# Optimization experiments

Measured on AMD Instinct MI355X. Metric: run time of the kernel, lower is better.

The kernel has to match this reference:

```python
import jax, jax.numpy as jnp
import numpy as np

B, DIM, H, W = 8, 128, 112, 112
WSZ, K = 7, 9
D4 = DIM // 4


def setup_inputs() -> dict:
    key = jax.random.key(0)
    ks = jax.random.split(key, 8)
    w = lambda k, shape: jax.random.normal(k, shape, jnp.float32) * 0.05
    return {
        'x_in': jax.random.normal(ks[0], (B, DIM, H, W), jnp.float32),
        'f_w': w(ks[1], (D4, DIM)), 'f_b': jnp.zeros((D4,), jnp.float32),
        'f_gn_w': jnp.ones((D4,), jnp.float32), 'f_gn_b': jnp.zeros((D4,), jnp.float32),
        'p_w': w(ks[2], (DIM, D4)), 'p_b': jnp.zeros((DIM,), jnp.float32),
        'p_gn_w': jnp.ones((DIM,), jnp.float32), 'p_gn_b': jnp.zeros((DIM,), jnp.float32),
        'r_w': w(ks[3], (DIM, DIM)), 'r_b': jnp.zeros((DIM,), jnp.float32),
        'r_gn_w': jnp.ones((DIM,), jnp.float32), 'r_gn_b': jnp.zeros((DIM,), jnp.float32),
        'e1_w': w(ks[4], (D4, 2 * D4)), 'e1_b': jnp.zeros((D4,), jnp.float32),
        'e2_w': w(ks[5], (1, D4)), 'e2_b': jnp.zeros((1,), jnp.float32),
        'gamma': jnp.ones((1,), jnp.float32), 'beta': jnp.zeros((1,), jnp.float32),
    }


def conv1x1(x, w, b):
    # 1x1 conv == channel matmul. x: (B,C,H,W), w: (O,C)
    return jnp.einsum('bchw,oc->bohw', x, w) + b[None, :, None, None]


def gn1(x, w, b, eps=1e-5):
    # GroupNorm(1, C): normalize over (C,H,W) per sample
    mu = x.mean(axis=(1, 2, 3), keepdims=True)
    var = x.var(axis=(1, 2, 3), keepdims=True)
    xn = (x - mu) * jax.lax.rsqrt(var + eps)
    return xn * w[None, :, None, None] + b[None, :, None, None]


def reference(x_in, f_w, f_b, f_gn_w, f_gn_b, p_w, p_b, p_gn_w, p_gn_b,
              r_w, r_b, r_gn_w, r_gn_b, e1_w, e1_b, e2_w, e2_b, gamma, beta):
    b, c, h, w_ = x_in.shape
    wg = hg = WSZ
    pw, ph = h // wg, w_ // hg  # per-window spatial dims (16,16)

    residual = gn1(conv1x1(x_in, r_w, r_b), r_gn_w, r_gn_b)

    # 'b c (Wg w) (Hg h) -> (b Wg Hg) c w h'
    x = x_in.reshape(b, c, wg, pw, hg, ph).transpose(0, 2, 4, 1, 3, 5)
    x = x.reshape(b * wg * hg, c, pw, ph)

    f = gn1(conv1x1(x, f_w, f_b), f_gn_w, f_gn_b)  # (Bp, D4, pw, ph)
    bp, c4, hp, wp = f.shape
    n = hp * wp

    xf = f.reshape(bp, c4, n).transpose(0, 2, 1)  # (Bp, N, C4) nodes

    gy, gx = jnp.meshgrid(jnp.arange(hp), jnp.arange(wp), indexing='ij')
    grid = jnp.stack([gy, gx], axis=-1).astype(jnp.float32).reshape(n, 2)
    grid = (grid - grid.mean(0)) / (grid.std(0, ddof=1) + 1e-5)  # torch std is unbiased

    xa = jnp.concatenate([xf, jnp.broadcast_to(grid, (bp, n, 2))], axis=-1)
    xn = xa / jnp.maximum(jnp.linalg.norm(xa, axis=-1, keepdims=True), 1e-8)
    sim = jnp.einsum('bnd,bmd->bnm', xn, xn)  # (Bp, N, N) cosine sim
    sim = jnp.where(jnp.eye(n, dtype=bool), -jnp.inf, sim)
    _, topk_idx = jax.lax.top_k(sim, K)  # (Bp, N, K)

    # gather neighbor messages; scatter_add back to row == sum over K (rows are dense)
    msg = jax.vmap(lambda a, i: a[i])(xf, topk_idx)          # (Bp, N, K, C4)
    src = jnp.broadcast_to(xf[:, :, None, :], msg.shape)      # (Bp, N, K, C4)
    ef = jnp.concatenate([src, msg], axis=-1)                 # (Bp, N, K, 2*C4)
    h1 = jax.nn.silu(ef @ e1_w.T + e1_b)
    wgt = jax.nn.sigmoid(h1 @ e2_w.T + e2_b)[..., 0]          # (Bp, N, K)
    out = (msg * wgt[..., None]).sum(axis=2)                  # (Bp, N, C4)

    out = out * gamma + xf * beta
    out = out.reshape(bp, hp, wp, c4).transpose(0, 3, 1, 2)   # (Bp, C4, hp, wp)

    # '(b Wg Hg) c w h -> b c (Wg w) (Hg h)'
    out = out.reshape(b, wg, hg, c4, hp, wp).transpose(0, 3, 1, 4, 2, 5)
    out = out.reshape(b, c4, h, w_)

    out = gn1(conv1x1(out, p_w, p_b), p_gn_w, p_gn_b) + residual
    return out
```

## Files before the change

### kernel.cpp

```cpp
#include <hip/hip_runtime.h>
#include <hip/hip_fp16.h>
#include <math.h>

#define CIN 128
#define C4  32
#define HW  12544
#define KNB 9
#define NWIN 392

__device__ inline double wave_sum(double v) {
#pragma unroll
    for (int off = 32; off; off >>= 1) v += __shfl_down(v, off);
    return v;
}

#define TOP9_INSERT(sv, mi, tv, ti)                                  \
    {                                                                \
        _Pragma("unroll")                                            \
        for (int j = KNB - 1; j >= 1; --j) {                         \
            bool cj  = (sv) > tv[j];                                 \
            bool cjm = (sv) > tv[j - 1];                             \
            tv[j] = cj ? (cjm ? tv[j - 1] : (sv)) : tv[j];           \
            ti[j] = cj ? (cjm ? ti[j - 1] : (mi)) : ti[j];           \
        }                                                            \
        bool c0 = (sv) > tv[0];                                      \
        tv[0] = c0 ? (sv) : tv[0];                                   \
        ti[0] = c0 ? (mi) : ti[0];                                   \
    }

__global__ __launch_bounds__(256) void prep_kernel(
    const float* __restrict__ f_w, const float* __restrict__ r_w,
    const float* __restrict__ p_w,
    double* __restrict__ fw64t, float* __restrict__ rwt_t, float* __restrict__ pwt_t)
{
    const int i = blockIdx.x * 256 + threadIdx.x;
    if (i < 4096)  fw64t[(i & 127) * 32 + (i >> 7)]  = (double)f_w[i];
    if (i < 16384) rwt_t[(i & 127) * 128 + (i >> 7)] = r_w[i];
    if (i < 4096)  pwt_t[(i & 31) * 128 + (i >> 5)]  = p_w[i];
}

__global__ __launch_bounds__(512, 2) void fconv_rstats_kernel(
    const float* __restrict__ x_in,
    const double* __restrict__ fw64t, const float* __restrict__ f_b,
    const float* __restrict__ f_gn_w, const float* __restrict__ f_gn_b,
    const float* __restrict__ rwt_t, const float* __restrict__ r_b,
    float* __restrict__ xfws, double* __restrict__ invnws,
    double* __restrict__ stats)
{
    __shared__ __align__(16) char smem[34944];
    double* vbuf = (double*)smem;
    double* red  = (double*)(smem + 34816);
    const int t = threadIdx.x;

    if (blockIdx.x < NWIN) {
        const int win = blockIdx.x;
        const int b = win / 49, wg = (win / 7) % 7, hg = win % 7;
        const int n = t & 255, s = t >> 8;
        const int py = n >> 4, px = n & 15;
        const int rs = __builtin_amdgcn_readfirstlane(s);

        const float* xb = x_in + (size_t)b * CIN * HW + (size_t)(wg * 16 + py) * 112 + (hg * 16 + px);
        const double* wB = fw64t + 16 * rs;
        double acc[16];
#pragma unroll
        for (int j = 0; j < 16; ++j) acc[j] = 0.0;
#pragma unroll 2
        for (int c = 0; c < CIN; ++c) {
            double xv = (double)xb[(size_t)c * HW];
            const double* wr = wB + c * 32;
#pragma unroll
            for (int j = 0; j < 16; ++j) acc[j] = fma(wr[j], xv, acc[j]);
        }
        double s1 = 0.0, s2 = 0.0;
#pragma unroll
        for (int j = 0; j < 16; ++j) {
            double v = acc[j] + (double)f_b[16 * rs + j];
            acc[j] = v; s1 += v; s2 += v * v;
        }
        s1 = wave_sum(s1); s2 = wave_sum(s2);
        {
            int w = t >> 6;
            if ((t & 63) == 0) { red[w] = s1; red[8 + w] = s2; }
        }
        __syncthreads();
        double rs1 = 0.0, rs2 = 0.0;
#pragma unroll
        for (int w = 0; w < 8; ++w) { rs1 += red[w]; rs2 += red[8 + w]; }
        const double mu   = rs1 * (1.0 / 8192.0);
        const double var  = rs2 * (1.0 / 8192.0) - mu * mu;
        const double rstd = 1.0 / sqrt(var + 1e-5);

        float myv[16];
#pragma unroll
        for (int j = 0; j < 16; ++j) {
            int c = 16 * rs + j;
            myv[j] = (float)((acc[j] - mu) * rstd * (double)f_gn_w[c] + (double)f_gn_b[c]);
        }
        float* xrow = xfws + (size_t)(win * 256 + n) * 36;
#pragma unroll
        for (int q4 = 0; q4 < 4; ++q4) {
            float4 f = { myv[4 * q4], myv[4 * q4 + 1], myv[4 * q4 + 2], myv[4 * q4 + 3] };
            ((float4*)(xrow + 16 * rs))[q4] = f;
        }
        const double ginv = 1.0 / (sqrt(5440.0 / 255.0) + 1e-5);
        const float gyf = (float)(((double)py - 7.5) * ginv);
        const float gxf = (float)(((double)px - 7.5) * ginv);
        if (s == 0) {
            float4 g4 = { gyf, gxf, 0.f, 0.f };
            ((float4*)(xrow + 32))[0] = g4;
        }
        if (s == 1) {
#pragma unroll
            for (int j = 0; j < 16; ++j) vbuf[n * 17 + j] = (double)myv[j];
        }
        __syncthreads();
        if (s == 0) {
            double nrm = 0.0;
#pragma unroll
            for (int j = 0; j < 16; ++j) { double x = (double)myv[j]; nrm += x * x; }
#pragma unroll
            for (int j = 0; j < 16; ++j) { double x = vbuf[n * 17 + j]; nrm += x * x; }
            double xg = (double)gyf; nrm += xg * xg;
            double xh = (double)gxf; nrm += xh * xh;
            invnws[win * 256 + n] = 1.0 / fmax(sqrt(nrm), 1e-8);
        }
    } else {
        const int idx = blockIdx.x - NWIN;
        const int b = idx / 98, rem = idx % 98;
        const int oc = rem / 49, pg = rem % 49;
        const int sh = t >> 8, n = t & 255;
        const int rsh = __builtin_amdgcn_readfirstlane(sh);
        const float* wR = rwt_t + oc * 64 + rsh * 32;
        const float* xb = x_in + (size_t)b * CIN * HW + pg * 256 + n;
        float acc[32];
#pragma unroll
        for (int o = 0; o < 32; ++o) acc[o] = r_b[oc * 64 + rsh * 32 + o];
#pragma unroll 2
        for (int c = 0; c < CIN; ++c) {
            float xv = xb[(size_t)c * HW];
            const float* wr = wR + c * 128;
#pragma unroll
            for (int o = 0; o < 32; ++o) acc[o] = fmaf(wr[o], xv, acc[o]);
        }
        double s1 = 0.0, s2 = 0.0;
#pragma unroll
        for (int o = 0; o < 32; ++o) { double v = (double)acc[o]; s1 += v; s2 += v * v; }
        s1 = wave_sum(s1); s2 = wave_sum(s2);
        {
            int w = t >> 6;
            if ((t & 63) == 0) { red[w] = s1; red[8 + w] = s2; }
        }
        __syncthreads();
        if (t == 0) {
            double a = 0.0, c = 0.0;
#pragma unroll
            for (int w = 0; w < 8; ++w) { a += red[w]; c += red[8 + w]; }
            atomicAdd(&stats[b * 4 + 0], a);
            atomicAdd(&stats[b * 4 + 1], c);
        }
    }
}

__global__ __launch_bounds__(256, 4) void sim_kernel(
    const float* __restrict__ xfws, const double* __restrict__ invnws,
    float* __restrict__ pval, short* __restrict__ pidx)
{
    const int bid = blockIdx.x;
    const int win = bid >> 2, m0 = (bid & 3) << 6;
    const int n = threadIdx.x;

    double xad[34];
    {
        const float4* own = (const float4*)(xfws + (size_t)(win * 256 + n) * 36);
#pragma unroll
        for (int q = 0; q < 8; ++q) {
            float4 f = own[q];
            xad[q * 4 + 0] = (double)f.x; xad[q * 4 + 1] = (double)f.y;
            xad[q * 4 + 2] = (double)f.z; xad[q * 4 + 3] = (double)f.w;
        }
        float4 g = own[8];
        xad[32] = (double)g.x; xad[33] = (double)g.y;
    }
    const double inv_self = invnws[(size_t)win * 256 + n];
    const float*  xmb  = xfws + (size_t)(win * 256 + m0) * 36;
    const double* invb = invnws + (size_t)win * 256 + m0;

    float tv[KNB]; int ti[KNB];
#pragma unroll
    for (int k = 0; k < KNB; ++k) { tv[k] = -INFINITY; ti[k] = 0; }
#pragma unroll 2
    for (int mm = 0; mm < 64; ++mm) {
        const float* xm = xmb + mm * 36;
        double d0 = 0.0, d1 = 0.0, d2 = 0.0, d3 = 0.0;
#pragma unroll
        for (int q = 0; q < 8; ++q) {
            d0 = fma((double)xm[4 * q + 0], xad[4 * q + 0], d0);
            d1 = fma((double)xm[4 * q + 1], xad[4 * q + 1], d1);
            d2 = fma((double)xm[4 * q + 2], xad[4 * q + 2], d2);
            d3 = fma((double)xm[4 * q + 3], xad[4 * q + 3], d3);
        }
        d0 = fma((double)xm[32], xad[32], d0);
        d1 = fma((double)xm[33], xad[33], d1);
        double d = (d0 + d1) + (d2 + d3);
        float sv = (float)(d * (inv_self * invb[mm]));
        sv = (m0 + mm == n) ? -INFINITY : sv;
        TOP9_INSERT(sv, m0 + mm, tv, ti);
    }
    const size_t base = ((size_t)bid * 256 + n) * 9;
#pragma unroll
    for (int k = 0; k < KNB; ++k) { pval[base + k] = tv[k]; pidx[base + k] = (short)ti[k]; }
}

__global__ __launch_bounds__(512, 2) void merge_mlp_kernel(
    const float* __restrict__ xfws,
    const float* __restrict__ pval, const short* __restrict__ pidx,
    const float* __restrict__ e1_w, const float* __restrict__ e1_b,
    const float* __restrict__ e2_w, const float* __restrict__ e2_b,
    const float* __restrict__ gamma, const float* __restrict__ beta,
    const float* __restrict__ pwt_t, const float* __restrict__ p_b,
    float* __restrict__ gnn, double* __restrict__ stats)
{
    __shared__ __align__(16) char smem[75136];
    float*   xf  = (float*)smem;
    __half2* hm2 = (__half2*)(smem + 33792);
    float*   hs  = (float*)(smem + 51200);
    float*   gnx = (float*)(smem + 51200);
    short*   Ti  = (short*)(smem + 68096);
    float*   Wt  = (float*)(smem + 70400);
    double*  red = (double*)(smem + 75008);

    const int bid = blockIdx.x;
    const int win = bid >> 1, half = bid & 1;
    const int b = win / 49, wg = (win / 7) % 7, hg = win % 7;
    const int t = threadIdx.x;
    const int nl = t & 127, s = t >> 7;
    const int gn = half * 128 + nl;
    const int rs = __builtin_amdgcn_readfirstlane(s);

    {
        const float* src = xfws + (size_t)win * 256 * 36;
        for (int i = t; i < 8192; i += 512)
            xf[(i >> 5) * 33 + (i & 31)] = src[(i >> 5) * 36 + (i & 31)];
    }
    __syncthreads();

    {
        float xr[C4];
#pragma unroll
        for (int c = 0; c < C4; ++c) xr[c] = xf[gn * 33 + c];
#pragma unroll
        for (int jj = 0; jj < 8; ++jj) {
            const int j = 8 * rs + jj;
            const float* w = e1_w + j * 64;
            float h0 = e1_b[j], h1 = 0.f;
#pragma unroll
            for (int c = 0; c < C4; c += 2) {
                h0 = fmaf(w[c], xr[c], h0);
                h1 = fmaf(w[c + 1], xr[c + 1], h1);
            }
            hs[nl * 33 + j] = h0 + h1;
        }
    }
    {
        const int mh = t & 255;
        const int rjh = __builtin_amdgcn_readfirstlane(t >> 8);
        float xr[C4];
#pragma unroll
        for (int c = 0; c < C4; ++c) xr[c] = xf[mh * 33 + c];
#pragma unroll
        for (int u = 0; u < 8; ++u) {
            const int j = 16 * rjh + 2 * u;
            const float* w0 = e1_w + j * 64 + 32;
            const float* w1 = e1_w + (j + 1) * 64 + 32;
            float a0 = 0.f, a1 = 0.f;
#pragma unroll
            for (int c = 0; c < C4; ++c) {
                a0 = fmaf(w0[c], xr[c], a0);
                a1 = fmaf(w1[c], xr[c], a1);
            }
            hm2[mh * 17 + 8 * rjh + u] = __floats2half2_rn(a0, a1);
        }
    }
    if (s == 0) {
        float tv[KNB]; int ti[KNB];
#pragma unroll
        for (int k = 0; k < KNB; ++k) { tv[k] = -INFINITY; ti[k] = 0; }
        for (int qd = 0; qd < 4; ++qd) {
            const size_t base = ((size_t)(win * 4 + qd) * 256 + gn) * 9;
#pragma unroll
            for (int k = 0; k < KNB; ++k) {
                float sv = pval[base + k];
                int   mi = (int)pidx[base + k];
                TOP9_INSERT(sv, mi, tv, ti);
            }
        }
#pragma unroll
        for (int k = 0; k < KNB; ++k) Ti[nl * 9 + k] = (short)ti[k];
    }
    __syncthreads();

    {
        float hsr[C4];
#pragma unroll
        for (int c = 0; c < C4; ++c) hsr[c] = hs[nl * 33 + c];
        const float e2b = e2_b[0];
        for (int k = s; k < KNB; k += 4) {
            const int m = (int)Ti[nl * 9 + k];
            float a2 = 0.f;
#pragma unroll
            for (int jp = 0; jp < 16; ++jp) {
                float2 hv = __half22float2(hm2[m * 17 + jp]);
                float h0 = hsr[2 * jp] + hv.x;
                float h1 = hsr[2 * jp + 1] + hv.y;
                float sg0 = 1.f / (1.f + __expf(-h0));
                a2 = fmaf(e2_w[2 * jp], h0 * sg0, a2);
                float sg1 = 1.f / (1.f + __expf(-h1));
                a2 = fmaf(e2_w[2 * jp + 1], h1 * sg1, a2);
            }
            Wt[nl * 9 + k] = 1.f / (1.f + __expf(-(a2 + e2b)));
        }
    }
    __syncthreads();

    {
        short tis[KNB]; float wks[KNB];
#pragma unroll
        for (int k = 0; k < KNB; ++k) { tis[k] = Ti[nl * 9 + k]; wks[k] = Wt[nl * 9 + k]; }
        const float g = gamma[0], be = beta[0];
        const int py = gn >> 4, px = gn & 15;
        float* gp = gnn + (size_t)b * C4 * HW + (size_t)(wg * 16 + py) * 112 + (hg * 16 + px);
#pragma unroll
        for (int cc = 0; cc < 8; ++cc) {
            const int c = 8 * rs + cc;
            float o = 0.f;
#pragma unroll
            for (int k = 0; k < KNB; ++k)
                o = fmaf(wks[k], xf[(int)tis[k] * 33 + c], o);
            float gl = fmaf(g, o, be * xf[gn * 33 + c]);
            gp[(size_t)c * HW] = gl;
            gnx[nl * 33 + c] = gl;
        }
    }
    __syncthreads();

    {
        float gr[C4];
#pragma unroll
        for (int c = 0; c < C4; ++c) gr[c] = gnx[nl * 33 + c];
        const int o0 = 32 * rs;
        float a[32];
#pragma unroll
        for (int o = 0; o < 32; ++o) a[o] = p_b[o0 + o];
#pragma unroll 2
        for (int c = 0; c < C4; ++c) {
            const float* w = pwt_t + c * 128 + o0;
#pragma unroll
            for (int o = 0; o < 32; ++o) a[o] = fmaf(w[o], gr[c], a[o]);
        }
        double s1 = 0.0, s2 = 0.0;
#pragma unroll
        for (int o = 0; o < 32; ++o) { double v = (double)a[o]; s1 += v; s2 += v * v; }
        s1 = wave_sum(s1); s2 = wave_sum(s2);
        int w = t >> 6;
        if ((t & 63) == 0) { red[w] = s1; red[8 + w] = s2; }
    }
    __syncthreads();
    if (t == 0) {
        double a = 0.0, c = 0.0;
#pragma unroll
        for (int w = 0; w < 8; ++w) { a += red[w]; c += red[8 + w]; }
        atomicAdd(&stats[b * 4 + 2], a);
        atomicAdd(&stats[b * 4 + 3], c);
    }
}

__global__ __launch_bounds__(256) void final_kernel(
    const float* __restrict__ x_in, const float* __restrict__ gnn,
    const float* __restrict__ rwt_t, const float* __restrict__ r_b,
    const float* __restrict__ r_gn_w, const float* __restrict__ r_gn_b,
    const float* __restrict__ pwt_t, const float* __restrict__ p_b,
    const float* __restrict__ p_gn_w, const float* __restrict__ p_gn_b,
    const double* __restrict__ stats,
    float* __restrict__ out)
{
    const int idx = blockIdx.x;
    const int b = idx / 196, rem = idx % 196;
    const int ocq = rem / 49, pg = rem % 49;
    const int t = threadIdx.x;

    const double NN = (double)CIN * HW;
    const double mu_r = stats[b * 4 + 0] / NN;
    const float  rs_r = (float)(1.0 / sqrt(stats[b * 4 + 1] / NN - mu_r * mu_r + 1e-5));
    const double mu_p = stats[b * 4 + 2] / NN;
    const float  rs_p = (float)(1.0 / sqrt(stats[b * 4 + 3] / NN - mu_p * mu_p + 1e-5));
    const float fmur = (float)mu_r, fmup = (float)mu_p;

    const int p = pg * 256 + t;
    const float* xb = x_in + (size_t)b * CIN * HW + p;
    const float* gb = gnn + (size_t)b * C4 * HW + p;
    float* ob = out + (size_t)b * CIN * HW + p;

    float xg[C4];
#pragma unroll
    for (int c = 0; c < C4; ++c) xg[c] = gb[(size_t)c * HW];

    float accR[32], accP[32];
#pragma unroll
    for (int o = 0; o < 32; ++o) {
        accR[o] = r_b[ocq * 32 + o];
        accP[o] = p_b[ocq * 32 + o];
    }
#pragma unroll 2
    for (int c = 0; c < CIN; ++c) {
        float xv = xb[(size_t)c * HW];
        const float* w = rwt_t + c * 128 + ocq * 32;
#pragma unroll
        for (int o = 0; o < 32; ++o) accR[o] = fmaf(w[o], xv, accR[o]);
    }
#pragma unroll
    for (int c = 0; c < C4; ++c) {
        const float* w = pwt_t + c * 128 + ocq * 32;
#pragma unroll
        for (int o = 0; o < 32; ++o) accP[o] = fmaf(w[o], xg[c], accP[o]);
    }
#pragma unroll
    for (int o = 0; o < 32; ++o) {
        const int O = ocq * 32 + o;
        float yr = (accR[o] - fmur) * rs_r * r_gn_w[O] + r_gn_b[O];
        float yp = (accP[o] - fmup) * rs_p * p_gn_w[O] + p_gn_b[O];
        ob[(size_t)O * HW] = yp + yr;
    }
}

extern "C" void kernel_launch(void* const* d_in, const int* in_sizes, int n_in,
                              void* d_out, int out_size, void* d_ws, size_t ws_size,
                              hipStream_t stream)
{
    const float* x_in   = (const float*)d_in[0];
    const float* f_w    = (const float*)d_in[1];
    const float* f_b    = (const float*)d_in[2];
    const float* f_gn_w = (const float*)d_in[3];
    const float* f_gn_b = (const float*)d_in[4];
    const float* p_w    = (const float*)d_in[5];
    const float* p_b    = (const float*)d_in[6];
    const float* p_gn_w = (const float*)d_in[7];
    const float* p_gn_b = (const float*)d_in[8];
    const float* r_w    = (const float*)d_in[9];
    const float* r_b    = (const float*)d_in[10];
    const float* r_gn_w = (const float*)d_in[11];
    const float* r_gn_b = (const float*)d_in[12];
    const float* e1_w   = (const float*)d_in[13];
    const float* e1_b   = (const float*)d_in[14];
    const float* e2_w   = (const float*)d_in[15];
    const float* e2_b   = (const float*)d_in[16];
    const float* gamma  = (const float*)d_in[17];
    const float* beta   = (const float*)d_in[18];

    char* wsb = (char*)d_ws;
    float*  gnn    = (float*) (wsb + 0);
    double* stats  = (double*)(wsb + 12845056);
    float*  xfws   = (float*) (wsb + 12845312);
    double* invnws = (double*)(wsb + 27296000);
    float*  pval   = (float*) (wsb + 28098816);
    short*  pidx   = (short*) (wsb + 42549504);
    double* fw64t  = (double*)(wsb + 49774848);
    float*  rwt_t  = (float*) (wsb + 49807616);
    float*  pwt_t  = (float*) (wsb + 49873152);

    hipMemsetAsync(stats, 0, 32 * sizeof(double), stream);
    prep_kernel<<<64, 256, 0, stream>>>(f_w, r_w, p_w, fw64t, rwt_t, pwt_t);
    fconv_rstats_kernel<<<NWIN + 784, 512, 0, stream>>>(
        x_in, fw64t, f_b, f_gn_w, f_gn_b, rwt_t, r_b, xfws, invnws, stats);
    sim_kernel<<<NWIN * 4, 256, 0, stream>>>(xfws, invnws, pval, pidx);
    merge_mlp_kernel<<<NWIN * 2, 512, 0, stream>>>(
        xfws, pval, pidx, e1_w, e1_b, e2_w, e2_b, gamma, beta, pwt_t, p_b, gnn, stats);
    final_kernel<<<1568, 256, 0, stream>>>(
        x_in, gnn, rwt_t, r_b, r_gn_w, r_gn_b, pwt_t, p_b, p_gn_w, p_gn_b, stats, (float*)d_out);
}
```

Before: 327.1 us.

## Split neighbor-MLP precompute into sim kernel and move p-conv stats to new kernel

The per-node half of the edge-MLP first layer (the message projection) now runs in extra blocks appended to the similarity kernel and is written to a half-precision workspace. The merge kernel stores features in fp16 shared memory, drops the p-conv statistics pass, and raises its occupancy target. A separate pstats kernel now reads gnn back to compute the GroupNorm statistics. Neighbor indices shrink to bytes. The aim is less shared memory and fewer registers per merge block so more blocks fit per CU, at the cost of an extra kernel launch, a reread of gnn, and fp16 rounding of the features and hidden activations.

```diff
diff --git a/kernel.cpp b/kernel.cpp
--- a/kernel.cpp
+++ b/kernel.cpp
@@ -39,7 +39,7 @@
     if (i < 4096)  pwt_t[(i & 31) * 128 + (i >> 5)]  = p_w[i];
 }
 
-__global__ __launch_bounds__(512, 2) void fconv_rstats_kernel(
+__global__ __launch_bounds__(512, 6) void fconv_rstats_kernel(
     const float* __restrict__ x_in,
     const double* __restrict__ fw64t, const float* __restrict__ f_b,
     const float* __restrict__ f_gn_w, const float* __restrict__ f_gn_b,
@@ -161,73 +161,101 @@
     }
 }
 
-__global__ __launch_bounds__(256, 4) void sim_kernel(
+__global__ __launch_bounds__(256, 4) void sim_hm_kernel(
     const float* __restrict__ xfws, const double* __restrict__ invnws,
-    float* __restrict__ pval, short* __restrict__ pidx)
+    const float* __restrict__ e1_w,
+    float* __restrict__ pval, unsigned char* __restrict__ pidx,
+    __half* __restrict__ hmws)
 {
     const int bid = blockIdx.x;
-    const int win = bid >> 2, m0 = (bid & 3) << 6;
-    const int n = threadIdx.x;
-
-    double xad[34];
-    {
-        const float4* own = (const float4*)(xfws + (size_t)(win * 256 + n) * 36);
+    if (bid < 4 * NWIN) {
+        const int win = bid >> 2, m0 = (bid & 3) << 6;
+        const int n = threadIdx.x;
+
+        double xad[34];
+        {
+            const float4* own = (const float4*)(xfws + (size_t)(win * 256 + n) * 36);
+#pragma unroll
+            for (int q = 0; q < 8; ++q) {
+                float4 f = own[q];
+                xad[q * 4 + 0] = (double)f.x; xad[q * 4 + 1] = (double)f.y;
+                xad[q * 4 + 2] = (double)f.z; xad[q * 4 + 3] = (double)f.w;
+            }
+            float4 g = own[8];
+            xad[32] = (double)g.x; xad[33] = (double)g.y;
+        }
+        const double inv_self = invnws[(size_t)win * 256 + n];
+        const float*  xmb  = xfws + (size_t)(win * 256 + m0) * 36;
+        const double* invb = invnws + (size_t)win * 256 + m0;
+
+        float tv[KNB]; int ti[KNB];
+#pragma unroll
+        for (int k = 0; k < KNB; ++k) { tv[k] = -INFINITY; ti[k] = 0; }
+#pragma unroll 2
+        for (int mm = 0; mm < 64; ++mm) {
+            const float* xm = xmb + mm * 36;
+            double d0 = 0.0, d1 = 0.0, d2 = 0.0, d3 = 0.0;
+#pragma unroll
+            for (int q = 0; q < 8; ++q) {
+                d0 = fma((double)xm[4 * q + 0], xad[4 * q + 0], d0);
+                d1 = fma((double)xm[4 * q + 1], xad[4 * q + 1], d1);
+                d2 = fma((double)xm[4 * q + 2], xad[4 * q + 2], d2);
+                d3 = fma((double)xm[4 * q + 3], xad[4 * q + 3], d3);
+            }
+            d0 = fma((double)xm[32], xad[32], d0);
+            d1 = fma((double)xm[33], xad[33], d1);
+            double d = (d0 + d1) + (d2 + d3);
+            float sv = (float)(d * (inv_self * invb[mm]));
+            sv = (m0 + mm == n) ? -INFINITY : sv;
+            TOP9_INSERT(sv, m0 + mm, tv, ti);
+        }
+        const size_t base = ((size_t)bid * 256 + n) * 9;
+#pragma unroll
+        for (int k = 0; k < KNB; ++k) { pval[base + k] = tv[k]; pidx[base + k] = (unsigned char)ti[k]; }
+    } else {
+        const int idxm = bid - 4 * NWIN;
+        const int win = idxm >> 1, half = idxm & 1;
+        const int t = threadIdx.x;
+        const int n = t & 127;
+        const int jh = __builtin_amdgcn_readfirstlane(t >> 7);
+        const int gn = half * 128 + n;
+        const float4* xr4 = (const float4*)(xfws + (size_t)(win * 256 + gn) * 36);
+        float xr[32];
 #pragma unroll
         for (int q = 0; q < 8; ++q) {
-            float4 f = own[q];
-            xad[q * 4 + 0] = (double)f.x; xad[q * 4 + 1] = (double)f.y;
-            xad[q * 4 + 2] = (double)f.z; xad[q * 4 + 3] = (double)f.w;
-        }
-        float4 g = own[8];
-        xad[32] = (double)g.x; xad[33] = (double)g.y;
-    }
-    const double inv_self = invnws[(size_t)win * 256 + n];
-    const float*  xmb  = xfws + (size_t)(win * 256 + m0) * 36;
-    const double* invb = invnws + (size_t)win * 256 + m0;
-
-    float tv[KNB]; int ti[KNB];
-#pragma unroll
-    for (int k = 0; k < KNB; ++k) { tv[k] = -INFINITY; ti[k] = 0; }
-#pragma unroll 2
-    for (int mm = 0; mm < 64; ++mm) {
-        const float* xm = xmb + mm * 36;
-        double d0 = 0.0, d1 = 0.0, d2 = 0.0, d3 = 0.0;
-#pragma unroll
-        for (int q = 0; q < 8; ++q) {
-            d0 = fma((double)xm[4 * q + 0], xad[4 * q + 0], d0);
-            d1 = fma((double)xm[4 * q + 1], xad[4 * q + 1], d1);
-            d2 = fma((double)xm[4 * q + 2], xad[4 * q + 2], d2);
-            d3 = fma((double)xm[4 * q + 3], xad[4 * q + 3], d3);
-        }
-        d0 = fma((double)xm[32], xad[32], d0);
-        d1 = fma((double)xm[33], xad[33], d1);
-        double d = (d0 + d1) + (d2 + d3);
-        float sv = (float)(d * (inv_self * invb[mm]));
-        sv = (m0 + mm == n) ? -INFINITY : sv;
-        TOP9_INSERT(sv, m0 + mm, tv, ti);
-    }
-    const size_t base = ((size_t)bid * 256 + n) * 9;
-#pragma unroll
-    for (int k = 0; k < KNB; ++k) { pval[base + k] = tv[k]; pidx[base + k] = (short)ti[k]; }
-}
-
-__global__ __launch_bounds__(512, 2) void merge_mlp_kernel(
-    const float* __restrict__ xfws,
-    const float* __restrict__ pval, const short* __restrict__ pidx,
+            float4 f = xr4[q];
+            xr[4 * q + 0] = f.x; xr[4 * q + 1] = f.y;
+            xr[4 * q + 2] = f.z; xr[4 * q + 3] = f.w;
+        }
+        __align__(16) __half hv[16];
+#pragma unroll
+        for (int jj = 0; jj < 16; ++jj) {
+            const float* w = e1_w + (16 * jh + jj) * 64 + 32;
+            float a = 0.f;
+#pragma unroll
+            for (int c = 0; c < C4; ++c) a = fmaf(w[c], xr[c], a);
+            hv[jj] = __float2half_rn(a);
+        }
+        float4* dst = (float4*)(hmws + (size_t)(win * 256 + gn) * 32 + 16 * jh);
+        dst[0] = ((const float4*)hv)[0];
+        dst[1] = ((const float4*)hv)[1];
+    }
+}
+
+__global__ __launch_bounds__(512, 6) void merge_mlp_kernel(
+    const float* __restrict__ xfws, const __half* __restrict__ hmws,
+    const float* __restrict__ pval, const unsigned char* __restrict__ pidx,
     const float* __restrict__ e1_w, const float* __restrict__ e1_b,
     const float* __restrict__ e2_w, const float* __restrict__ e2_b,
     const float* __restrict__ gamma, const float* __restrict__ beta,
-    const float* __restrict__ pwt_t, const float* __restrict__ p_b,
-    float* __restrict__ gnn, double* __restrict__ stats)
-{
-    __shared__ __align__(16) char smem[75136];
-    float*   xf  = (float*)smem;
-    __half2* hm2 = (__half2*)(smem + 33792);
-    float*   hs  = (float*)(smem + 51200);
-    float*   gnx = (float*)(smem + 51200);
-    short*   Ti  = (short*)(smem + 68096);
-    float*   Wt  = (float*)(smem + 70400);
-    double*  red = (double*)(smem + 75008);
+    float* __restrict__ gnn)
+{
+    __shared__ __align__(16) char smem[50432];
+    __half2* xf2 = (__half2*)smem;
+    __half2* hm2 = (__half2*)(smem + 17408);
+    __half2* hs2 = (__half2*)(smem + 34816);
+    short*   Ti  = (short*)(smem + 43520);
+    float*   Wt  = (float*)(smem + 45824);
 
     const int bid = blockIdx.x;
     const int win = bid >> 1, half = bid & 1;
@@ -238,16 +266,30 @@
     const int rs = __builtin_amdgcn_readfirstlane(s);
 
     {
-        const float* src = xfws + (size_t)win * 256 * 36;
-        for (int i = t; i < 8192; i += 512)
-            xf[(i >> 5) * 33 + (i & 31)] = src[(i >> 5) * 36 + (i & 31)];
+        const int r = t >> 1, hh = t & 1;
+        const float4* sx = (const float4*)(xfws + (size_t)win * 9216 + r * 36 + hh * 16);
+#pragma unroll
+        for (int q = 0; q < 4; ++q) {
+            float4 f = sx[q];
+            xf2[r * 17 + hh * 8 + 2 * q]     = __floats2half2_rn(f.x, f.y);
+            xf2[r * 17 + hh * 8 + 2 * q + 1] = __floats2half2_rn(f.z, f.w);
+        }
+        const uint4* sh = (const uint4*)(hmws + (size_t)win * 8192 + r * 32 + hh * 16);
+        uint4 u0 = sh[0], u1 = sh[1];
+        unsigned int* d = (unsigned int*)(hm2 + r * 17 + hh * 8);
+        d[0] = u0.x; d[1] = u0.y; d[2] = u0.z; d[3] = u0.w;
+        d[4] = u1.x; d[5] = u1.y; d[6] = u1.z; d[7] = u1.w;
     }
     __syncthreads();
 
     {
         float xr[C4];
 #pragma unroll
-        for (int c = 0; c < C4; ++c) xr[c] = xf[gn * 33 + c];
+        for (int q = 0; q < 16; ++q) {
+            float2 f = __half22float2(xf2[gn * 17 + q]);
+            xr[2 * q] = f.x; xr[2 * q + 1] = f.y;
+        }
+        float hsv[8];
 #pragma unroll
         for (int jj = 0; jj < 8; ++jj) {
             const int j = 8 * rs + jj;
@@ -258,28 +300,11 @@
                 h0 = fmaf(w[c], xr[c], h0);
                 h1 = fmaf(w[c + 1], xr[c + 1], h1);
             }
-            hs[nl * 33 + j] = h0 + h1;
-        }
-    }
-    {
-        const int mh = t & 255;
-        const int rjh = __builtin_amdgcn_readfirstlane(t >> 8);
-        float xr[C4];
-#pragma unroll
-        for (int c = 0; c < C4; ++c) xr[c] = xf[mh * 33 + c];
-#pragma unroll
-        for (int u = 0; u < 8; ++u) {
-            const int j = 16 * rjh + 2 * u;
-            const float* w0 = e1_w + j * 64 + 32;
-            const float* w1 = e1_w + (j + 1) * 64 + 32;
-            float a0 = 0.f, a1 = 0.f;
-#pragma unroll
-            for (int c = 0; c < C4; ++c) {
-                a0 = fmaf(w0[c], xr[c], a0);
-                a1 = fmaf(w1[c], xr[c], a1);
-            }
-            hm2[mh * 17 + 8 * rjh + u] = __floats2half2_rn(a0, a1);
-        }
+            hsv[jj] = h0 + h1;
+        }
+#pragma unroll
+        for (int u = 0; u < 4; ++u)
+            hs2[nl * 17 + 4 * rs + u] = __floats2half2_rn(hsv[2 * u], hsv[2 * u + 1]);
     }
     if (s == 0) {
         float tv[KNB]; int ti[KNB];
@@ -302,7 +327,10 @@
     {
         float hsr[C4];
 #pragma unroll
-        for (int c = 0; c < C4; ++c) hsr[c] = hs[nl * 33 + c];
+        for (int q = 0; q < 16; ++q) {
+            float2 f = __half22float2(hs2[nl * 17 + q]);
+            hsr[2 * q] = f.x; hsr[2 * q + 1] = f.y;
+        }
         const float e2b = e2_b[0];
         for (int k = s; k < KNB; k += 4) {
             const int m = (int)Ti[nl * 9 + k];
@@ -329,38 +357,61 @@
         const float g = gamma[0], be = beta[0];
         const int py = gn >> 4, px = gn & 15;
         float* gp = gnn + (size_t)b * C4 * HW + (size_t)(wg * 16 + py) * 112 + (hg * 16 + px);
+        float xo[8];
+#pragma unroll
+        for (int q = 0; q < 4; ++q) {
+            float2 f = __half22float2(xf2[gn * 17 + 4 * rs + q]);
+            xo[2 * q] = f.x; xo[2 * q + 1] = f.y;
+        }
+        float o[8];
+#pragma unroll
+        for (int cc = 0; cc < 8; ++cc) o[cc] = 0.f;
+#pragma unroll
+        for (int k = 0; k < KNB; ++k) {
+            const int mrow = (int)tis[k] * 17 + 4 * rs;
+#pragma unroll
+            for (int q = 0; q < 4; ++q) {
+                float2 mv = __half22float2(xf2[mrow + q]);
+                o[2 * q]     = fmaf(wks[k], mv.x, o[2 * q]);
+                o[2 * q + 1] = fmaf(wks[k], mv.y, o[2 * q + 1]);
+            }
+        }
 #pragma unroll
         for (int cc = 0; cc < 8; ++cc) {
-            const int c = 8 * rs + cc;
-            float o = 0.f;
-#pragma unroll
-            for (int k = 0; k < KNB; ++k)
-                o = fmaf(wks[k], xf[(int)tis[k] * 33 + c], o);
-            float gl = fmaf(g, o, be * xf[gn * 33 + c]);
-            gp[(size_t)c * HW] = gl;
-            gnx[nl * 33 + c] = gl;
-        }
-    }
-    __syncthreads();
-
+            float gl = fmaf(g, o[cc], be * xo[cc]);
+            gp[(size_t)(8 * rs + cc) * HW] = gl;
+        }
+    }
+}
+
+__global__ __launch_bounds__(256, 8) void pstats_kernel(
+    const float* __restrict__ gnn, const float* __restrict__ p_w,
+    const float* __restrict__ p_b, double* __restrict__ stats)
+{
+    __shared__ double red[16];
+    const int idx = blockIdx.x;
+    const int b = idx / 98, pg = idx % 98;
+    const int t = threadIdx.x;
+    const int pix = pg * 128 + (t & 127);
+    const int oh = __builtin_amdgcn_readfirstlane(t >> 7);
+
+    const float* gb = gnn + (size_t)b * C4 * HW + pix;
+    float g[C4];
+#pragma unroll
+    for (int c = 0; c < C4; ++c) g[c] = gb[(size_t)c * HW];
+
+    double s1 = 0.0, s2 = 0.0;
+    const float* pwb = p_w + (size_t)oh * 64 * C4;
+#pragma unroll 4
+    for (int o = 0; o < 64; ++o) {
+        const float* w = pwb + o * C4;
+        float y = p_b[oh * 64 + o];
+#pragma unroll
+        for (int c = 0; c < C4; ++c) y = fmaf(w[c], g[c], y);
+        s1 += (double)y; s2 += (double)y * (double)y;
+    }
+    s1 = wave_sum(s1); s2 = wave_sum(s2);
     {
-        float gr[C4];
-#pragma unroll
-        for (int c = 0; c < C4; ++c) gr[c] = gnx[nl * 33 + c];
-        const int o0 = 32 * rs;
-        float a[32];
-#pragma unroll
-        for (int o = 0; o < 32; ++o) a[o] = p_b[o0 + o];
-#pragma unroll 2
-        for (int c = 0; c < C4; ++c) {
-            const float* w = pwt_t + c * 128 + o0;
-#pragma unroll
-            for (int o = 0; o < 32; ++o) a[o] = fmaf(w[o], gr[c], a[o]);
-        }
-        double s1 = 0.0, s2 = 0.0;
-#pragma unroll
-        for (int o = 0; o < 32; ++o) { double v = (double)a[o]; s1 += v; s2 += v * v; }
-        s1 = wave_sum(s1); s2 = wave_sum(s2);
         int w = t >> 6;
         if ((t & 63) == 0) { red[w] = s1; red[8 + w] = s2; }
     }
@@ -368,7 +419,7 @@
     if (t == 0) {
         double a = 0.0, c = 0.0;
 #pragma unroll
-        for (int w = 0; w < 8; ++w) { a += red[w]; c += red[8 + w]; }
+        for (int w = 0; w < 4; ++w) { a += red[w]; c += red[8 + w]; }
         atomicAdd(&stats[b * 4 + 2], a);
         atomicAdd(&stats[b * 4 + 3], c);
     }
@@ -457,23 +508,26 @@
     const float* beta   = (const float*)d_in[18];
 
     char* wsb = (char*)d_ws;
-    float*  gnn    = (float*) (wsb + 0);
-    double* stats  = (double*)(wsb + 12845056);
-    float*  xfws   = (float*) (wsb + 12845312);
-    double* invnws = (double*)(wsb + 27296000);
-    float*  pval   = (float*) (wsb + 28098816);
-    short*  pidx   = (short*) (wsb + 42549504);
-    double* fw64t  = (double*)(wsb + 49774848);
-    float*  rwt_t  = (float*) (wsb + 49807616);
-    float*  pwt_t  = (float*) (wsb + 49873152);
+    float*         gnn    = (float*)        (wsb + 0);
+    double*        stats  = (double*)       (wsb + 12845056);
+    float*         xfws   = (float*)        (wsb + 12845312);
+    double*        invnws = (double*)       (wsb + 27296000);
+    float*         pval   = (float*)        (wsb + 28098816);
+    unsigned char* pidx   = (unsigned char*)(wsb + 42549504);
+    double*        fw64t  = (double*)       (wsb + 46162176);
+    float*         rwt_t  = (float*)        (wsb + 46194944);
+    float*         pwt_t  = (float*)        (wsb + 46260480);
+    __half*        hmws   = (__half*)       (wsb + 46276864);
 
     hipMemsetAsync(stats, 0, 32 * sizeof(double), stream);
     prep_kernel<<<64, 256, 0, stream>>>(f_w, r_w, p_w, fw64t, rwt_t, pwt_t);
     fconv_rstats_kernel<<<NWIN + 784, 512, 0, stream>>>(
         x_in, fw64t, f_b, f_gn_w, f_gn_b, rwt_t, r_b, xfws, invnws, stats);
-    sim_kernel<<<NWIN * 4, 256, 0, stream>>>(xfws, invnws, pval, pidx);
+    sim_hm_kernel<<<NWIN * 4 + NWIN * 2, 256, 0, stream>>>(
+        xfws, invnws, e1_w, pval, pidx, hmws);
     merge_mlp_kernel<<<NWIN * 2, 512, 0, stream>>>(
-        xfws, pval, pidx, e1_w, e1_b, e2_w, e2_b, gamma, beta, pwt_t, p_b, gnn, stats);
+        xfws, hmws, pval, pidx, e1_w, e1_b, e2_w, e2_b, gamma, beta, gnn);
+    pstats_kernel<<<784, 256, 0, stream>>>(gnn, p_w, p_b, stats);
     final_kernel<<<1568, 256, 0, stream>>>(
         x_in, gnn, rwt_t, r_b, r_gn_w, r_gn_b, pwt_t, p_b, p_gn_w, p_gn_b, stats, (float*)d_out);
 }
```

New measurement: 327.4 us. About the same (+0.1%).
